# Kernel optimization log

Measured on AMD Instinct MI355X. Metric: run time of the kernel, lower is better.

Reference implementation:

```python
import jax, jax.numpy as jnp
import numpy as np

B, N, L = 16, 128, 512            # batch, scan length, per-step feature (= configs.seq_len)
D, S, K, R, H = 1024, 16, 4, 64, 2048  # d_model, d_state, ker_size, dt_rank, hidden_dimention


def _mamba_params(key, scale=0.02):
    ks = jax.random.split(key, 6)
    return dict(
        in_w=jax.random.normal(ks[0], (2 * D, L)) * scale,
        conv_w=jax.random.normal(ks[1], (D, K)) * scale,
        conv_b=jnp.zeros((D,)),
        xproj_w=jax.random.normal(ks[2], (R + 2 * S, D)) * scale,
        dt_w=jax.random.normal(ks[3], (D, R)) * scale,
        dt_b=jax.random.normal(ks[4], (D,)) * scale,
        A_log=jnp.tile(jnp.log(jnp.arange(1, S + 1, dtype=jnp.float32)), (D, 1)),
        Dp=jnp.ones((D,)),
        out_w=jax.random.normal(ks[5], (L, D)) * scale,
    )


def setup_inputs():
    key = jax.random.key(0)
    kx, kf, kr, k1, k2 = jax.random.split(key, 5)
    inp = {"x": jax.random.normal(kx, (B, N, L), dtype=jnp.float32)}
    for pre, k in (("f_", kf), ("r_", kr)):
        for n, v in _mamba_params(k).items():
            inp[pre + n] = v
    inp["pu_w"] = jax.random.normal(k1, (H, L)) * 0.02
    inp["pu_b"] = jnp.zeros((H,))
    inp["pl_w"] = jax.random.normal(k2, (L, H)) * 0.02
    inp["pl_b"] = jnp.zeros((L,))
    inp["ln_g"] = jnp.ones((L,))
    inp["ln_b"] = jnp.zeros((L,))
    return inp


def _ln(x, g, b, eps=1e-5):
    m = x.mean(-1, keepdims=True)
    v = ((x - m) ** 2).mean(-1, keepdims=True)
    return (x - m) * jax.lax.rsqrt(v + eps) * g + b


def _dw_causal_conv(x, w, b):
    # x: [B,N,D]; depthwise causal conv along N with kernel [D,K]
    xt = jnp.pad(x.transpose(0, 2, 1), ((0, 0), (0, 0), (K - 1, 0)))  # [B,D,N+K-1]
    y = jax.lax.conv_general_dilated(xt, w[:, None, :], (1,), 'VALID',
                                     dimension_numbers=('NCH', 'OIH', 'NCH'),
                                     feature_group_count=D)
    return (y + b[None, :, None]).transpose(0, 2, 1)


def _mamba(x, in_w, conv_w, conv_b, xproj_w, dt_w, dt_b, A_log, Dp, out_w):
    # standard Mamba block (in_proj -> depthwise conv -> silu -> selective scan -> gate -> out_proj)
    xi, res = jnp.split(x @ in_w.T, 2, axis=-1)             # [B,N,D] each
    xc = jax.nn.silu(_dw_causal_conv(xi, conv_w, conv_b))   # [B,N,D]
    dbc = xc @ xproj_w.T                                    # [B,N,R+2S]
    dt, Bm, Cm = dbc[..., :R], dbc[..., R:R + S], dbc[..., R + S:]
    delta = jax.nn.softplus(dt @ dt_w.T + dt_b)             # [B,N,D]
    A = -jnp.exp(A_log)                                     # [D,S]
    dA = jnp.exp(delta[..., None] * A)                      # [B,N,D,S]
    dBx = delta[..., None] * Bm[:, :, None, :] * xc[..., None]

    def step(h, t):
        dA_t, dBx_t, C_t = t
        h = dA_t * h + dBx_t                                # [B,D,S]
        return h, jnp.einsum('bds,bs->bd', h, C_t)

    _, ys = jax.lax.scan(step, jnp.zeros((x.shape[0], D, S), x.dtype),
                         (dA.transpose(1, 0, 2, 3), dBx.transpose(1, 0, 2, 3), Cm.transpose(1, 0, 2)))
    y = ys.transpose(1, 0, 2) + xc * Dp                     # [B,N,D]
    y = y * jax.nn.silu(res)
    return y @ out_w.T                                      # [B,N,L]


def reference(x, f_in_w, f_conv_w, f_conv_b, f_xproj_w, f_dt_w, f_dt_b, f_A_log, f_Dp, f_out_w,
              r_in_w, r_conv_w, r_conv_b, r_xproj_w, r_dt_w, r_dt_b, r_A_log, r_Dp, r_out_w,
              pu_w, pu_b, pl_w, pl_b, ln_g, ln_b):
    y1 = _mamba(x, f_in_w, f_conv_w, f_conv_b, f_xproj_w, f_dt_w, f_dt_b, f_A_log, f_Dp, f_out_w)
    y2 = _mamba(x[:, ::-1, :], r_in_w, r_conv_w, r_conv_b, r_xproj_w, r_dt_w, r_dt_b, r_A_log, r_Dp, r_out_w)
    y3 = _ln(x + y1 + y2[:, ::-1, :], ln_g, ln_b)
    yp = jax.nn.relu(y3 @ pu_w.T + pu_b)
    yp = yp @ pl_w.T + pl_b
    return _ln(yp + y3, ln_g, ln_b)
```

## Files before the change

kernel.cpp:

```cpp
#include <hip/hip_runtime.h>
#include <hip/hip_bf16.h>
#include <cstdint>

typedef __hip_bfloat16 bf16;

constexpr int Bb = 16, Nn = 128, Ll = 512, Dd = 1024, Ss = 16, Rr = 64, Hh = 2048;
constexpr int Mm = Bb * Nn;
#define LOG2E 1.44269504088896340736f

using bf16x8 = __attribute__((ext_vector_type(8))) __bf16;
using bf16x4 = __attribute__((ext_vector_type(4))) __bf16;
using f32x4  = __attribute__((ext_vector_type(4))) float;

__device__ __forceinline__ float to_f(float x) { return x; }
__device__ __forceinline__ float to_f(bf16 x) { return __bfloat162float(x); }
__device__ __forceinline__ void store_t(float* p, float v) { *p = v; }
__device__ __forceinline__ void store_t(bf16* p, float v) { *p = __float2bfloat16(v); }
__device__ __forceinline__ __bf16 cvt1(float x) {
  bf16 h = __float2bfloat16(x);
  return *reinterpret_cast<__bf16*>(&h);
}
__device__ __forceinline__ float bfraw_to_f(__bf16 x) {
  bf16 h = *reinterpret_cast<bf16*>(&x);
  return __bfloat162float(h);
}
__device__ __forceinline__ bf16x8 load8(const bf16* p) { return *(const bf16x8*)p; }
__device__ __forceinline__ bf16x8 load8(const float* p) {
  float4 a = *(const float4*)p;
  float4 b = *(const float4*)(p + 4);
  bf16x8 r;
  r[0] = cvt1(a.x); r[1] = cvt1(a.y); r[2] = cvt1(a.z); r[3] = cvt1(a.w);
  r[4] = cvt1(b.x); r[5] = cvt1(b.y); r[6] = cvt1(b.z); r[7] = cvt1(b.w);
  return r;
}
__device__ __forceinline__ bf16x8 load8rt(const void* p, size_t idx, int isbf) {
  if (isbf) return load8((const bf16*)p + idx);
  return load8((const float*)p + idx);
}
__device__ __forceinline__ float ldf(const void* p, int i, int isbf) {
  if (isbf) return __bfloat162float(((const bf16*)p)[i]);
  return ((const float*)p)[i];
}
__device__ __forceinline__ void gld16(const bf16* g, __bf16* l) {
  __builtin_amdgcn_global_load_lds(
      (const __attribute__((address_space(1))) void*)g,
      (__attribute__((address_space(3))) void*)l, 16, 0, 0);
}

enum { EPI_STORE = 0, EPI_BIAS_RELU = 1, EPI_ADD = 3, EPI_BIAS = 4, EPI_BIAS_SOFTPLUS = 5,
       EPI_ATOMIC = 6 };

__global__ void sniff_kernel(const unsigned short* __restrict__ xs, int* __restrict__ flags) {
  const int tid = threadIdx.x;
  int cnt = 0;
  for (int j = 0; j < 64; ++j) {
    int i = tid + j * 256;
    unsigned short u = xs[(size_t)i * 64];
    bf16 h = *reinterpret_cast<bf16*>(&u);
    float v = __bfloat162float(h);
    float a = fabsf(v);
    if (v == 0.f || (a > 0.0009765625f && a < 16.f)) ++cnt;
  }
  __shared__ int sc[256];
  sc[tid] = cnt;
  __syncthreads();
  for (int o = 128; o > 0; o >>= 1) {
    if (tid < o) sc[tid] += sc[tid + o];
    __syncthreads();
  }
  if (tid == 0) flags[0] = (sc[0] > 8192) ? 1 : 0;
}

__global__ __launch_bounds__(256) void prep_kernel(
    const int* __restrict__ flagp, const void* __restrict__ x,
    float* __restrict__ ZB, unsigned short* __restrict__ Xb,
    float* __restrict__ zerop,
    const void* __restrict__ fin, const void* __restrict__ rin,
    const void* __restrict__ fout, const void* __restrict__ rout,
    const void* __restrict__ puw, const void* __restrict__ plw,
    bf16* __restrict__ WBin, bf16* __restrict__ WBout,
    bf16* __restrict__ WBpu, bf16* __restrict__ WBpl) {
  const int isbf = *flagp;
  const int i = blockIdx.x * 256 + threadIdx.x;
  if (i < 262144) {
    float4 o;
    ushort4 u;
    if (isbf) {
      u = ((const ushort4*)x)[i];
      bf16 h0 = *reinterpret_cast<bf16*>(&u.x), h1 = *reinterpret_cast<bf16*>(&u.y);
      bf16 h2 = *reinterpret_cast<bf16*>(&u.z), h3 = *reinterpret_cast<bf16*>(&u.w);
      o = float4{__bfloat162float(h0), __bfloat162float(h1),
                 __bfloat162float(h2), __bfloat162float(h3)};
    } else {
      o = ((const float4*)x)[i];
      bf16 h0 = __float2bfloat16(o.x), h1 = __float2bfloat16(o.y);
      bf16 h2 = __float2bfloat16(o.z), h3 = __float2bfloat16(o.w);
      u = ushort4{*(unsigned short*)&h0, *(unsigned short*)&h1,
                  *(unsigned short*)&h2, *(unsigned short*)&h3};
    }
    ((float4*)ZB)[i] = o;
    ((ushort4*)Xb)[i] = u;
  } else if (i < 622592) {
    ((float4*)zerop)[i - 262144] = float4{0.f, 0.f, 0.f, 0.f};
  } else {
    const int j = i - 622592;
    const void* src;
    bf16* dst;
    int si;
    if (j < 131072) { src = fin; si = j; dst = WBin + (size_t)si * 8; }
    else if (j < 262144) { src = rin; si = j - 131072; dst = WBin + (size_t)1048576 + (size_t)si * 8; }
    else if (j < 393216) { src = puw; si = j - 262144; dst = WBpu + (size_t)si * 8; }
    else if (j < 524288) { src = plw; si = j - 393216; dst = WBpl + (size_t)si * 8; }
    else if (j < 589824) {
      src = fout; si = j - 524288;
      int e = si * 8;
      dst = WBout + (size_t)(e >> 10) * 2048 + (e & 1023);
    } else {
      src = rout; si = j - 589824;
      int e = si * 8;
      dst = WBout + (size_t)(e >> 10) * 2048 + 1024 + (e & 1023);
    }
    *(bf16x8*)dst = load8rt(src, (size_t)si * 8, isbf);
  }
}

constexpr int LDT2 = 72;

template <typename TC, int EPI>
__global__ __launch_bounds__(256) void gemm_rt(
    const int* __restrict__ flagp,
    const void* __restrict__ A, int lda, int abf,
    const void* __restrict__ Bw, const void* __restrict__ Bw2, int ldb,
    int bmode, int bsplit,
    TC* __restrict__ C, int ldc,
    const void* __restrict__ bias, const void* __restrict__ bias2,
    int N, int Kchunk, int zk, size_t a_doff, size_t c_doff) {
  const int isbf = *flagp;
  const int ab = (abf == 2) ? isbf : abf;
  __shared__ __align__(16) __bf16 As[64 * LDT2];
  __shared__ __align__(16) __bf16 Bs[64 * LDT2];
  const int tid = threadIdx.x;
  const int wave = tid >> 6, lane = tid & 63;
  const int quad = lane >> 4, l16 = lane & 15;
  const int wm = wave & 1, wn = wave >> 1;
  int bx = blockIdx.x, by = blockIdx.y;
  const int gx = gridDim.x, gy = gridDim.y;
  if ((gx & 7) == 0) {
    int id = bx + gx * by;
    int xcd = id & 7, sl = id >> 3;
    by = sl % gy;
    bx = (sl / gy) * 8 + xcd;
  }
  int zsl = blockIdx.z;
  const void* Ap = A;
  const void* Bp0 = Bw;
  const void* biasp = bias;
  if (bmode == 3) {
    const int dir = zsl / zk;
    zsl = zsl % zk;
    if (dir) {
      Ap = (const char*)A + a_doff * (size_t)(ab ? 2 : 4);
      C += c_doff;
      Bp0 = Bw2;
      biasp = bias2;
    }
  }
  const int m0 = by * 64, n0 = bx * 64;
  const int kb = zsl * Kchunk;
  const int srow = tid >> 3;
  const int scol = (tid & 7) * 8;
  f32x4 acc[2][2] = {};
  for (int k0 = kb; k0 < kb + Kchunk; k0 += 64) {
#pragma unroll
    for (int h = 0; h < 2; ++h) {
      int r = srow + h * 32;
      *(bf16x8*)(&As[r * LDT2 + scol]) =
          load8rt(Ap, (size_t)(m0 + r) * lda + k0 + scol, ab);
      int rb = n0 + r;
      rb = rb < N ? rb : N - 1;
      size_t bi = (size_t)rb * ldb + k0 + scol;
      *(bf16x8*)(&Bs[r * LDT2 + scol]) = load8rt(Bp0, bi, isbf);
    }
    __syncthreads();
#pragma unroll
    for (int kk2 = 0; kk2 < 2; ++kk2) {
      bf16x8 af[2], bfr[2];
#pragma unroll
      for (int i = 0; i < 2; ++i)
        af[i] = *(const bf16x8*)(&As[(wm * 32 + i * 16 + l16) * LDT2 + kk2 * 32 + quad * 8]);
#pragma unroll
      for (int j = 0; j < 2; ++j)
        bfr[j] = *(const bf16x8*)(&Bs[(wn * 32 + j * 16 + l16) * LDT2 + kk2 * 32 + quad * 8]);
#pragma unroll
      for (int i = 0; i < 2; ++i)
#pragma unroll
        for (int j = 0; j < 2; ++j)
          acc[i][j] = __builtin_amdgcn_mfma_f32_16x16x32_bf16(af[i], bfr[j], acc[i][j], 0, 0, 0);
    }
    __syncthreads();
  }
#pragma unroll
  for (int i = 0; i < 2; ++i) {
#pragma unroll
    for (int j = 0; j < 2; ++j) {
      const int col = n0 + wn * 32 + j * 16 + l16;
      if (col >= N) continue;
      float bv = 0.f;
      if (EPI == EPI_BIAS_RELU || EPI == EPI_BIAS || EPI == EPI_BIAS_SOFTPLUS)
        bv = ldf(biasp, col, isbf);
#pragma unroll
      for (int r = 0; r < 4; ++r) {
        const int row = m0 + wm * 32 + i * 16 + quad * 4 + r;
        size_t idx = (size_t)row * ldc + col;
        float v = acc[i][j][r];
        if (EPI == EPI_STORE) store_t(&C[idx], v);
        else if (EPI == EPI_BIAS_RELU) { v += bv; store_t(&C[idx], v > 0.f ? v : 0.f); }
        else if (EPI == EPI_BIAS) store_t(&C[idx], v + bv);
        else if (EPI == EPI_BIAS_SOFTPLUS) {
          v += bv;
          store_t(&C[idx], (v > 20.f) ? v : log1pf(__expf(v)));
        } else if (EPI == EPI_ATOMIC) {
          atomicAdd((float*)&C[idx], v);
        }
      }
    }
  }
}

template <typename TC, int EPI>
__global__ __launch_bounds__(256) void gemm128n(
    const int* __restrict__ flagp,
    const bf16* __restrict__ A, int lda,
    const bf16* __restrict__ Bw, int ldb,
    TC* __restrict__ C, int ldc,
    const void* __restrict__ bias,
    int Kchunk) {
  __shared__ __align__(16) __bf16 As[2][128 * 64];
  __shared__ __align__(16) __bf16 Bs[2][128 * 64];
  const int tid = threadIdx.x;
  const int wave = tid >> 6, lane = tid & 63;
  const int quad = lane >> 4, l16 = lane & 15;
  const int wr = wave >> 1, wc = wave & 1;
  int bx = blockIdx.x, by = blockIdx.y;
  const int gx = gridDim.x, gy = gridDim.y;
  if ((gx & 7) == 0) {
    int id = bx + gx * by;
    int xcd = id & 7, sl = id >> 3;
    by = sl % gy;
    bx = (sl / gy) * 8 + xcd;
  }
  const int m0 = by * 128, n0 = bx * 128;
  const int kb = blockIdx.z * Kchunk;
  const int kend = kb + Kchunk;
  const int lr = lane >> 3;
  const int lc = (lane & 7) * 8;
  auto STAGE = [&](int buf, int k0) {
#pragma unroll
    for (int rr = 0; rr < 4; ++rr) {
      const int rowb = rr * 32 + wave * 8;
      gld16(A + (size_t)(m0 + rowb + lr) * lda + k0 + lc, &As[buf][rowb * 64]);
      gld16(Bw + (size_t)(n0 + rowb + lr) * ldb + k0 + lc, &Bs[buf][rowb * 64]);
    }
  };
  f32x4 acc[4][4] = {};
  int cur = 0;
  STAGE(0, kb);
  __syncthreads();
  for (int k0 = kb; k0 < kend; k0 += 64) {
    if (k0 + 64 < kend) STAGE(cur ^ 1, k0 + 64);
#pragma unroll
    for (int kk = 0; kk < 2; ++kk) {
      bf16x8 af[4], bfr[4];
#pragma unroll
      for (int i = 0; i < 4; ++i)
        af[i] = *(const bf16x8*)(&As[cur][(wr * 64 + i * 16 + l16) * 64 + kk * 32 + quad * 8]);
#pragma unroll
      for (int j = 0; j < 4; ++j)
        bfr[j] = *(const bf16x8*)(&Bs[cur][(wc * 64 + j * 16 + l16) * 64 + kk * 32 + quad * 8]);
#pragma unroll
      for (int i = 0; i < 4; ++i)
#pragma unroll
        for (int j = 0; j < 4; ++j)
          acc[i][j] = __builtin_amdgcn_mfma_f32_16x16x32_bf16(af[i], bfr[j], acc[i][j], 0, 0, 0);
    }
    __syncthreads();
    cur ^= 1;
  }
  const int isbf = *flagp;
#pragma unroll
  for (int i = 0; i < 4; ++i) {
#pragma unroll
    for (int j = 0; j < 4; ++j) {
      const int col = n0 + wc * 64 + j * 16 + l16;
      float bv = 0.f;
      if (EPI == EPI_BIAS_RELU) bv = ldf(bias, col, isbf);
#pragma unroll
      for (int r = 0; r < 4; ++r) {
        const int row = m0 + wr * 64 + i * 16 + quad * 4 + r;
        size_t idx = (size_t)row * ldc + col;
        float v = acc[i][j][r];
        if (EPI == EPI_STORE) store_t(&C[idx], v);
        else if (EPI == EPI_BIAS_RELU) { v += bv; store_t(&C[idx], v > 0.f ? v : 0.f); }
        else if (EPI == EPI_ATOMIC) atomicAdd((float*)&C[idx], v);
      }
    }
  }
}

__global__ __launch_bounds__(256) void conv_silu_rt(
    const int* __restrict__ flagp, const bf16* __restrict__ X2b,
    const void* __restrict__ fcw, const void* __restrict__ fcb,
    const void* __restrict__ rcw, const void* __restrict__ rcb,
    bf16* __restrict__ XCb) {
  const int isbf = *flagp;
  const int dir = blockIdx.y >> 2;
  const int d = (blockIdx.y & 3) * 256 + threadIdx.x;
  const int m = blockIdx.x;
  const int t = m & (Nn - 1);
  const void* cw = dir ? rcw : fcw;
  const void* cb = dir ? rcb : fcb;
  float w0 = ldf(cw, d * 4 + 0, isbf), w1 = ldf(cw, d * 4 + 1, isbf);
  float w2 = ldf(cw, d * 4 + 2, isbf), w3 = ldf(cw, d * 4 + 3, isbf);
  float a = ldf(cb, d, isbf);
  const size_t base = (size_t)m * 4096 + (size_t)dir * 2048 + d;
  if (dir == 0) {
    if (t >= 3) a += w0 * to_f(X2b[base - 3 * 4096]);
    if (t >= 2) a += w1 * to_f(X2b[base - 2 * 4096]);
    if (t >= 1) a += w2 * to_f(X2b[base - 1 * 4096]);
    a += w3 * to_f(X2b[base]);
  } else {
    if (t + 3 < Nn) a += w0 * to_f(X2b[base + 3 * 4096]);
    if (t + 2 < Nn) a += w1 * to_f(X2b[base + 2 * 4096]);
    if (t + 1 < Nn) a += w2 * to_f(X2b[base + 1 * 4096]);
    a += w3 * to_f(X2b[base]);
  }
  const float s = a / (1.f + __builtin_amdgcn_exp2f(-a * LOG2E));
  XCb[(size_t)m * 2048 + (size_t)dir * 1024 + d] = __float2bfloat16(s);
}

__global__ __launch_bounds__(256) void scan_gate5(
    const int* __restrict__ flagp,
    const float* __restrict__ DBC0, bf16* __restrict__ XCb, const bf16* __restrict__ X2b,
    const bf16* __restrict__ DELTA0,
    const void* __restrict__ fAlog, const void* __restrict__ fDp,
    const void* __restrict__ rAlog, const void* __restrict__ rDp) {
  const int isbf = *flagp;
  const int dir = blockIdx.z;
  const float* DBC = DBC0 + (size_t)dir * Mm * 96;
  const bf16* DELTA = DELTA0 + (size_t)dir * Mm * 1024;
  const void* A_log = dir ? rAlog : fAlog;
  const void* Dp = dir ? rDp : fDp;
  __shared__ __align__(16) __bf16 sBC[Nn * 32];
  __shared__ __align__(16) __bf16 sD[Nn * 32];
  __shared__ __align__(16) __bf16 sX[Nn * 32];
  __shared__ __align__(16) __bf16 sG[Nn * 32];
  const int b = blockIdx.x;
  const int d0 = blockIdx.y * 32;
  const int tid = threadIdx.x;
  const size_t rowbase = (size_t)b * Nn;
  const size_t xc_col = (size_t)dir * 1024;
#pragma unroll
  for (int k = 0; k < 4; ++k) {
    int idx = tid + k * 256;
    int t = idx >> 3, c = idx & 7;
    float4 v = *(const float4*)(DBC + (rowbase + t) * 96 + 64 + c * 4);
    const int isC = (c >= 4) ? 2 : 0;
    const int cb4 = (c & 3) * 4;
    float vv[4] = {v.x, v.y, v.z, v.w};
#pragma unroll
    for (int e = 0; e < 4; ++e) {
      int s = cb4 + e;
      sBC[t * 32 + (s >> 1) * 4 + isC + (s & 1)] = cvt1(vv[e]);
    }
  }
#pragma unroll
  for (int k = 0; k < 2; ++k) {
    int idx = tid + k * 256;
    int t = idx >> 2, h = idx & 3;
    *(uint4*)&sD[t * 32 + h * 8] =
        *(const uint4*)(DELTA + (rowbase + t) * 1024 + d0 + h * 8);
    *(uint4*)&sX[t * 32 + h * 8] =
        *(const uint4*)(XCb + (rowbase + t) * 2048 + xc_col + d0 + h * 8);
    bf16x8 rv = *(const bf16x8*)(X2b + (rowbase + t) * 4096 + (size_t)dir * 2048 + 1024 + d0 + h * 8);
    bf16x8 gv;
#pragma unroll
    for (int e = 0; e < 8; ++e) {
      float r = bfraw_to_f(rv[e]);
      gv[e] = cvt1(r / (1.f + __builtin_amdgcn_exp2f(-r * LOG2E)));
    }
    *(bf16x8*)&sG[t * 32 + h * 8] = gv;
  }
  __syncthreads();
  const int wv = tid >> 6, lane = tid & 63;
  const int dl = lane & 7, sgp = lane >> 3;
  const int d_local = wv * 8 + dl;
  const int d = d0 + d_local;
  float A0 = -__expf(ldf(A_log, d * Ss + sgp * 2 + 0, isbf)) * LOG2E;
  float A1 = -__expf(ldf(A_log, d * Ss + sgp * 2 + 1, isbf)) * LOG2E;
  const float dp = ldf(Dp, d, isbf);
  float h0 = 0.f, h1 = 0.f;
  for (int pg = 0; pg < Nn / 4; ++pg) {
    float accs[4], xvs[4];
#pragma unroll
    for (int u = 0; u < 4; ++u) {
      const int p = pg * 4 + u;
      const int t = dir ? (Nn - 1 - p) : p;
      const float dv = bfraw_to_f(sD[t * 32 + d_local]);
      const float xv = bfraw_to_f(sX[t * 32 + d_local]);
      bf16x4 bc = *(const bf16x4*)&sBC[t * 32 + sgp * 4];
      const float dx = dv * xv;
      h0 = __builtin_amdgcn_exp2f(dv * A0) * h0 + dx * bfraw_to_f(bc[0]);
      h1 = __builtin_amdgcn_exp2f(dv * A1) * h1 + dx * bfraw_to_f(bc[1]);
      accs[u] = h0 * bfraw_to_f(bc[2]) + h1 * bfraw_to_f(bc[3]);
      xvs[u] = xv;
    }
#pragma unroll
    for (int u = 0; u < 4; ++u) {
      float a = accs[u];
      a += __shfl_xor(a, 8, 64);
      a += __shfl_xor(a, 16, 64);
      a += __shfl_xor(a, 32, 64);
      if (sgp == 0) {
        const int p = pg * 4 + u;
        const int t = dir ? (Nn - 1 - p) : p;
        const float g = bfraw_to_f(sG[t * 32 + d_local]);
        XCb[(rowbase + t) * 2048 + xc_col + d] = __float2bfloat16((a + xvs[u] * dp) * g);
      }
    }
  }
}

template <int MODE>
__global__ __launch_bounds__(256) void ln_rt(const int* __restrict__ flagp,
                                             const float* __restrict__ Z,
                                             const float* __restrict__ Zadd,
                                             const void* __restrict__ g,
                                             const void* __restrict__ bb,
                                             const void* __restrict__ pb,
                                             void* __restrict__ outp,
                                             bf16* __restrict__ outp2) {
  const int isbf = *flagp;
  const int row = blockIdx.x;
  const int tid = threadIdx.x;
  const int c0 = tid * 2;
  const float2* z = (const float2*)(Z + (size_t)row * Ll);
  float2 v = z[tid];
  if (MODE == 1) {
    const float2* za = (const float2*)(Zadd + (size_t)row * Ll);
    float2 a = za[tid];
    v.x += a.x + ldf(pb, c0, isbf);
    v.y += a.y + ldf(pb, c0 + 1, isbf);
  }
  float s = v.x + v.y, q = v.x * v.x + v.y * v.y;
#pragma unroll
  for (int o = 32; o > 0; o >>= 1) {
    s += __shfl_xor(s, o, 64);
    q += __shfl_xor(q, o, 64);
  }
  __shared__ float ss[4], qq[4];
  const int wv = tid >> 6, ln = tid & 63;
  if (ln == 0) { ss[wv] = s; qq[wv] = q; }
  __syncthreads();
  s = ss[0] + ss[1] + ss[2] + ss[3];
  q = qq[0] + qq[1] + qq[2] + qq[3];
  const float mean = s * (1.f / Ll);
  const float var = q * (1.f / Ll) - mean * mean;
  const float rs = rsqrtf(var + 1e-5f);
  const float o0 = (v.x - mean) * rs * ldf(g, c0, isbf) + ldf(bb, c0, isbf);
  const float o1 = (v.y - mean) * rs * ldf(g, c0 + 1, isbf) + ldf(bb, c0 + 1, isbf);
  if (MODE == 0) {
    float* out = (float*)outp;
    out[(size_t)row * Ll + c0] = o0;
    out[(size_t)row * Ll + c0 + 1] = o1;
    outp2[(size_t)row * Ll + c0] = __float2bfloat16(o0);
    outp2[(size_t)row * Ll + c0 + 1] = __float2bfloat16(o1);
  } else {
    if (isbf) {
      bf16* out = (bf16*)outp;
      out[(size_t)row * Ll + c0] = __float2bfloat16(o0);
      out[(size_t)row * Ll + c0 + 1] = __float2bfloat16(o1);
    } else {
      float* out = (float*)outp;
      out[(size_t)row * Ll + c0] = o0;
      out[(size_t)row * Ll + c0 + 1] = o1;
    }
  }
}

extern "C" void kernel_launch(void* const* d_in, const int* in_sizes, int n_in, void* d_out,
                              int out_size, void* d_ws, size_t ws_size, hipStream_t stream) {
  char* ws = (char*)d_ws;
  int* flags = (int*)ws;
  bf16* X2b = (bf16*)(ws + 256);
  bf16* XCb = X2b + (size_t)Mm * 4096;
  bf16* Y3b = XCb + (size_t)Mm * 2048;
  bf16* DELTA = Y3b + (size_t)Mm * 512;
  bf16* Xb = DELTA + (size_t)2 * Mm * 1024;
  bf16* WBin = Xb + (size_t)Mm * 512;
  bf16* WBout = WBin + (size_t)4096 * 512;
  bf16* WBpu = WBout + (size_t)512 * 2048;
  bf16* WBpl = WBpu + (size_t)2048 * 512;
  float* DBC = (float*)(WBpl + (size_t)512 * 2048);
  float* Z2 = DBC + (size_t)2 * Mm * 96;
  float* ZB = Z2 + (size_t)Mm * 512;
  float* Y3 = ZB + (size_t)Mm * 512;
  bf16* H1 = X2b;
  size_t needed = 256 +
                  2 * ((size_t)Mm * 4096 + (size_t)Mm * 2048 + (size_t)Mm * 512 +
                       (size_t)2 * Mm * 1024 + (size_t)Mm * 512 +
                       (size_t)4096 * 512 + (size_t)512 * 2048 +
                       (size_t)2048 * 512 + (size_t)512 * 2048) +
                  4 * ((size_t)2 * Mm * 96 + (size_t)3 * Mm * 512);
  if (ws_size < needed) return;

  const void* x = d_in[0];
  const dim3 blk(256);

  sniff_kernel<<<dim3(1), blk, 0, stream>>>((const unsigned short*)x, flags);
  prep_kernel<<<dim3(4992), blk, 0, stream>>>(
      flags, x, ZB, (unsigned short*)Xb, DBC,
      d_in[1], d_in[10], d_in[9], d_in[18], d_in[19], d_in[21],
      WBin, WBout, WBpu, WBpl);
  gemm128n<bf16, EPI_STORE><<<dim3(32, 16), blk, 0, stream>>>(
      flags, Xb, Ll, WBin, Ll, X2b, 4096, nullptr, Ll);
  conv_silu_rt<<<dim3(Mm, 8), blk, 0, stream>>>(flags, X2b, d_in[2], d_in[3],
                                                d_in[11], d_in[12], XCb);
  gemm_rt<float, EPI_ATOMIC><<<dim3(2, 32, 8), blk, 0, stream>>>(
      flags, XCb, 2048, 1, d_in[4], d_in[13], Dd, 3, 0,
      DBC, 96, nullptr, nullptr, 96, 256, 4, 1024, (size_t)Mm * 96);
  gemm_rt<bf16, EPI_BIAS_SOFTPLUS><<<dim3(16, 32, 2), blk, 0, stream>>>(
      flags, DBC, 96, 0, d_in[5], d_in[14], Rr, 3, 0,
      DELTA, 1024, d_in[6], d_in[15], 1024, Rr, 1, (size_t)Mm * 96, (size_t)Mm * 1024);
  scan_gate5<<<dim3(Bb, Dd / 32, 2), blk, 0, stream>>>(
      flags, DBC, XCb, X2b, DELTA, d_in[7], d_in[8], d_in[16], d_in[17]);
  gemm128n<float, EPI_ATOMIC><<<dim3(4, 16, 4), blk, 0, stream>>>(
      flags, XCb, 2048, WBout, 2048, ZB, Ll, nullptr, Ll);
  ln_rt<0><<<dim3(Mm), blk, 0, stream>>>(flags, ZB, nullptr, d_in[23], d_in[24], nullptr,
                                         (void*)Y3, Y3b);
  gemm128n<bf16, EPI_BIAS_RELU><<<dim3(16, 16), blk, 0, stream>>>(
      flags, Y3b, Ll, WBpu, Ll, H1, Hh, d_in[20], Ll);
  gemm128n<float, EPI_ATOMIC><<<dim3(4, 16, 4), blk, 0, stream>>>(
      flags, H1, Hh, WBpl, 2048, Z2, Ll, nullptr, Ll);
  ln_rt<1><<<dim3(Mm), blk, 0, stream>>>(flags, Z2, Y3, d_in[23], d_in[24], d_in[22],
                                         d_out, nullptr);

  (void)in_sizes; (void)n_in; (void)out_size;
}
```

Before: 320.4 us.

## Interleave delta/x in scan LDS, use permlane32 swap, double split-K

The scan kernel now stores delta and xc interleaved in a single shared buffer, so each step reads one bf16 pair instead of two separate LDS loads. Where the builtin is available, the cross-half wave reduction uses permlane32_swap instead of a shuffle. The two atomic split-K output GEMMs go from 4 to 8 K-splits, with the chunk size cut from 512 to 256, to launch more blocks. The extra splits add more atomic traffic to the fp32 accumulators.

Result: slower. 357.8 us (+11.7%).

```diff
diff --git a/kernel.cpp b/kernel.cpp
--- a/kernel.cpp
+++ b/kernel.cpp
@@ -10,6 +10,7 @@
 
 using bf16x8 = __attribute__((ext_vector_type(8))) __bf16;
 using bf16x4 = __attribute__((ext_vector_type(4))) __bf16;
+using bf16x2 = __attribute__((ext_vector_type(2))) __bf16;
 using f32x4  = __attribute__((ext_vector_type(4))) float;
 
 __device__ __forceinline__ float to_f(float x) { return x; }
@@ -338,7 +339,7 @@
   XCb[(size_t)m * 2048 + (size_t)dir * 1024 + d] = __float2bfloat16(s);
 }
 
-__global__ __launch_bounds__(256) void scan_gate5(
+__global__ __launch_bounds__(256) void scan_gate6(
     const int* __restrict__ flagp,
     const float* __restrict__ DBC0, bf16* __restrict__ XCb, const bf16* __restrict__ X2b,
     const bf16* __restrict__ DELTA0,
@@ -351,8 +352,7 @@
   const void* A_log = dir ? rAlog : fAlog;
   const void* Dp = dir ? rDp : fDp;
   __shared__ __align__(16) __bf16 sBC[Nn * 32];
-  __shared__ __align__(16) __bf16 sD[Nn * 32];
-  __shared__ __align__(16) __bf16 sX[Nn * 32];
+  __shared__ __align__(16) __bf16 sDX[Nn * 64];
   __shared__ __align__(16) __bf16 sG[Nn * 32];
   const int b = blockIdx.x;
   const int d0 = blockIdx.y * 32;
@@ -377,10 +377,16 @@
   for (int k = 0; k < 2; ++k) {
     int idx = tid + k * 256;
     int t = idx >> 2, h = idx & 3;
-    *(uint4*)&sD[t * 32 + h * 8] =
-        *(const uint4*)(DELTA + (rowbase + t) * 1024 + d0 + h * 8);
-    *(uint4*)&sX[t * 32 + h * 8] =
-        *(const uint4*)(XCb + (rowbase + t) * 2048 + xc_col + d0 + h * 8);
+    bf16x8 dv8 = *(const bf16x8*)(DELTA + (rowbase + t) * 1024 + d0 + h * 8);
+    bf16x8 xv8 = *(const bf16x8*)(XCb + (rowbase + t) * 2048 + xc_col + d0 + h * 8);
+    bf16x8 lo, hi;
+#pragma unroll
+    for (int e = 0; e < 4; ++e) {
+      lo[2 * e] = dv8[e];     lo[2 * e + 1] = xv8[e];
+      hi[2 * e] = dv8[e + 4]; hi[2 * e + 1] = xv8[e + 4];
+    }
+    *(bf16x8*)&sDX[t * 64 + h * 16] = lo;
+    *(bf16x8*)&sDX[t * 64 + h * 16 + 8] = hi;
     bf16x8 rv = *(const bf16x8*)(X2b + (rowbase + t) * 4096 + (size_t)dir * 2048 + 1024 + d0 + h * 8);
     bf16x8 gv;
 #pragma unroll
@@ -405,8 +411,9 @@
     for (int u = 0; u < 4; ++u) {
       const int p = pg * 4 + u;
       const int t = dir ? (Nn - 1 - p) : p;
-      const float dv = bfraw_to_f(sD[t * 32 + d_local]);
-      const float xv = bfraw_to_f(sX[t * 32 + d_local]);
+      bf16x2 dx2 = *(const bf16x2*)&sDX[t * 64 + d_local * 2];
+      const float dv = bfraw_to_f(dx2[0]);
+      const float xv = bfraw_to_f(dx2[1]);
       bf16x4 bc = *(const bf16x4*)&sBC[t * 32 + sgp * 4];
       const float dx = dv * xv;
       h0 = __builtin_amdgcn_exp2f(dv * A0) * h0 + dx * bfraw_to_f(bc[0]);
@@ -419,7 +426,16 @@
       float a = accs[u];
       a += __shfl_xor(a, 8, 64);
       a += __shfl_xor(a, 16, 64);
+#if __has_builtin(__builtin_amdgcn_permlane32_swap)
+      {
+        unsigned au = __builtin_bit_cast(unsigned, a);
+        auto pr = __builtin_amdgcn_permlane32_swap(au, au, false, false);
+        float other = __builtin_bit_cast(float, (lane & 32) ? pr[0] : pr[1]);
+        a += other;
+      }
+#else
       a += __shfl_xor(a, 32, 64);
+#endif
       if (sgp == 0) {
         const int p = pg * 4 + u;
         const int t = dir ? (Nn - 1 - p) : p;
@@ -531,16 +547,16 @@
   gemm_rt<bf16, EPI_BIAS_SOFTPLUS><<<dim3(16, 32, 2), blk, 0, stream>>>(
       flags, DBC, 96, 0, d_in[5], d_in[14], Rr, 3, 0,
       DELTA, 1024, d_in[6], d_in[15], 1024, Rr, 1, (size_t)Mm * 96, (size_t)Mm * 1024);
-  scan_gate5<<<dim3(Bb, Dd / 32, 2), blk, 0, stream>>>(
+  scan_gate6<<<dim3(Bb, Dd / 32, 2), blk, 0, stream>>>(
       flags, DBC, XCb, X2b, DELTA, d_in[7], d_in[8], d_in[16], d_in[17]);
-  gemm128n<float, EPI_ATOMIC><<<dim3(4, 16, 4), blk, 0, stream>>>(
-      flags, XCb, 2048, WBout, 2048, ZB, Ll, nullptr, Ll);
+  gemm128n<float, EPI_ATOMIC><<<dim3(4, 16, 8), blk, 0, stream>>>(
+      flags, XCb, 2048, WBout, 2048, ZB, Ll, nullptr, 256);
   ln_rt<0><<<dim3(Mm), blk, 0, stream>>>(flags, ZB, nullptr, d_in[23], d_in[24], nullptr,
                                          (void*)Y3, Y3b);
   gemm128n<bf16, EPI_BIAS_RELU><<<dim3(16, 16), blk, 0, stream>>>(
       flags, Y3b, Ll, WBpu, Ll, H1, Hh, d_in[20], Ll);
-  gemm128n<float, EPI_ATOMIC><<<dim3(4, 16, 4), blk, 0, stream>>>(
-      flags, H1, Hh, WBpl, 2048, Z2, Ll, nullptr, Ll);
+  gemm128n<float, EPI_ATOMIC><<<dim3(4, 16, 8), blk, 0, stream>>>(
+      flags, H1, Hh, WBpl, 2048, Z2, Ll, nullptr, 256);
   ln_rt<1><<<dim3(Mm), blk, 0, stream>>>(flags, Z2, Y3, d_in[23], d_in[24], d_in[22],
                                          d_out, nullptr);
 
```
